# Optimization experiments

Hardware: AMD Instinct MI355X
Metric: run time of the kernel (lower is better)

The kernel has to match this reference:

```python
import jax, jax.numpy as jnp
import numpy as np

N_HEAD = 16
N_KV = 4
HEAD_DIM = 128
EPS = 1e-6


def setup_inputs() -> dict:
    key = jax.random.key(0)
    k1, k2, k3 = jax.random.split(key, 3)
    d_model = N_HEAD * HEAD_DIM
    qkv_out = (N_HEAD + 2 * N_KV) * HEAD_DIM
    B, T = 2, 2048
    x = jax.random.normal(k1, (B, T, d_model), dtype=jnp.float32)
    W_qkv = jax.random.normal(k2, (d_model, qkv_out), dtype=jnp.float32) * (d_model ** -0.5)
    W_proj = jax.random.normal(k3, (d_model, d_model), dtype=jnp.float32) * (d_model ** -0.5)
    q_scale = jnp.ones((HEAD_DIM,), dtype=jnp.float32)
    k_scale = jnp.ones((HEAD_DIM,), dtype=jnp.float32)
    return {"x": x, "W_qkv": W_qkv, "W_proj": W_proj, "q_scale": q_scale, "k_scale": k_scale}


def _rms_norm(t):
    return t * jax.lax.rsqrt(jnp.mean(t * t, axis=-1, keepdims=True) + EPS)


def reference(x, W_qkv, W_proj, q_scale, k_scale):
    B, T, C = x.shape
    qkv = x @ W_qkv  # [B, T, (H+2*KV)*D]
    q, k, v = jnp.split(qkv, [N_HEAD * HEAD_DIM, (N_HEAD + N_KV) * HEAD_DIM], axis=-1)
    q = q.reshape(B, T, N_HEAD, HEAD_DIM).transpose(0, 2, 1, 3)  # [B,H,T,D]
    k = k.reshape(B, T, N_KV, HEAD_DIM).transpose(0, 2, 1, 3)    # [B,KV,T,D]
    v = v.reshape(B, T, N_KV, HEAD_DIM).transpose(0, 2, 1, 3)
    # QK RMS-norm with learned per-dim scales
    q = _rms_norm(q) * q_scale
    k = _rms_norm(k) * k_scale
    # GQA: repeat kv heads to match query heads
    rep = N_HEAD // N_KV
    k = jnp.repeat(k, rep, axis=1)
    v = jnp.repeat(v, rep, axis=1)
    # causal SDPA
    scale = 1.0 / jnp.sqrt(jnp.float32(HEAD_DIM))
    scores = jnp.einsum('bhqd,bhkd->bhqk', q, k) * scale
    causal = jnp.tril(jnp.ones((T, T), dtype=bool))
    scores = jnp.where(causal, scores, jnp.finfo(scores.dtype).min)
    attn = jax.nn.softmax(scores, axis=-1)
    y = jnp.einsum('bhqk,bhkd->bhqd', attn, v)  # [B,H,T,D]
    y = y.transpose(0, 2, 1, 3).reshape(B, T, C)
    return y @ W_proj
```

## Files before the change

### kernel.cpp

```cpp
#include <hip/hip_runtime.h>

typedef __bf16 bf16;
typedef __bf16 bf16x8 __attribute__((ext_vector_type(8)));
typedef __bf16 bf16x4 __attribute__((ext_vector_type(4)));
typedef float f32x4 __attribute__((ext_vector_type(4)));
typedef float f32x16 __attribute__((ext_vector_type(16)));
typedef unsigned u32x4 __attribute__((ext_vector_type(4)));

#define EXP2F(x) __builtin_amdgcn_exp2f(x)

#define LOAD_LDS16(gp, lp)                                                     \
  __builtin_amdgcn_global_load_lds(                                            \
      (const __attribute__((address_space(1))) void*)(gp),                     \
      (__attribute__((address_space(3))) void*)(lp), 16, 0, 0)

__global__ __launch_bounds__(256) void k_cvt_x(const float* __restrict__ in,
                                               bf16* __restrict__ out, int n4) {
  int i = blockIdx.x * 256 + threadIdx.x;
  if (i < n4) {
    float4 v = ((const float4*)in)[i];
    bf16x4 o = {(bf16)v.x, (bf16)v.y, (bf16)v.z, (bf16)v.w};
    ((bf16x4*)out)[i] = o;
  }
}

__global__ __launch_bounds__(256) void k_transpose(const float* __restrict__ in,
                                                   bf16* __restrict__ out,
                                                   int R, int C) {
  __shared__ bf16 t[64 * 65];
  int tid = threadIdx.x;
  int c0 = blockIdx.x * 64, r0 = blockIdx.y * 64;
#pragma unroll
  for (int i = 0; i < 16; ++i) {
    int f = i * 256 + tid;
    int rl = f >> 6, cl = f & 63;
    t[rl * 65 + cl] = (bf16)in[(size_t)(r0 + rl) * C + c0 + cl];
  }
  __syncthreads();
#pragma unroll
  for (int i = 0; i < 16; ++i) {
    int f = i * 256 + tid;
    int cl = f >> 6, rl = f & 63;
    out[(size_t)(c0 + cl) * R + r0 + rl] = t[rl * 65 + cl];
  }
}

template <typename OutT, int BM>
__global__ __launch_bounds__(512, 2) void k_gemm256(const bf16* __restrict__ A,
                                                    const bf16* __restrict__ Bt,
                                                    OutT* __restrict__ C,
                                                    int M, int N, int K) {
  constexpr int ASZ = 4 * BM * 8;
  constexpr int MREP = BM / 32;
  __shared__ alignas(16) bf16 As[2][2][ASZ];
  __shared__ alignas(16) bf16 Bs[2][2][4 * 256 * 8];
  int tid = threadIdx.x;
  int wid = tid >> 6, lane = tid & 63;
  int g = lane >> 4, lr = lane & 15;
  int wrow = (wid >> 2) * (BM / 2), wcol = (wid & 3) * 64;
  int gx = gridDim.x;
  int flat = blockIdx.y * gx + blockIdx.x;
  int cpx = (gx * gridDim.y) >> 3;
  int f2 = (flat & 7) * cpx + (flat >> 3);
  int row0 = (f2 % gx) * BM, col0 = (f2 / gx) * 256;
  int NT = K >> 6;
  f32x4 acc[MREP][4] = {};

  auto stageA = [&](int buf, int kh, int kt) {
#pragma unroll
    for (int pass = 0; pass < BM / 128; ++pass) {
      int slot = pass * 512 + tid;
      int kseg, row;
      if constexpr (BM == 256) { kseg = slot >> 8; row = slot & 255; }
      else { kseg = slot >> 7; row = slot & 127; }
      LOAD_LDS16(A + (size_t)(row0 + row) * K + kt * 64 + kh * 32 + kseg * 8,
                 &As[buf][kh][slot * 8]);
    }
  };
  auto stageB = [&](int buf, int kh, int kt) {
#pragma unroll
    for (int pass = 0; pass < 2; ++pass) {
      int slot = pass * 512 + tid;
      int kseg = slot >> 8, row = slot & 255;
      LOAD_LDS16(Bt + (size_t)(col0 + row) * K + kt * 64 + kh * 32 + kseg * 8,
                 &Bs[buf][kh][slot * 8]);
    }
  };
  auto dsA = [&](int buf, int s, int mq, bf16x8* af) {
#pragma unroll
    for (int i = 0; i < 4; ++i)
      af[i] = *(const bf16x8*)&As[buf][s]
                  [(g * BM + wrow + (mq * 4 + i) * 16 + lr) * 8];
  };
  auto dsB = [&](int buf, int s, bf16x8* bfr) {
#pragma unroll
    for (int i = 0; i < 4; ++i)
      bfr[i] = *(const bf16x8*)&Bs[buf][s][((g << 8) + wcol + i * 16 + lr) * 8];
  };
  auto mfma16 = [&](int mq, bf16x8* af, bf16x8* bfr) {
    __builtin_amdgcn_s_setprio(1);
#pragma unroll
    for (int i = 0; i < 4; ++i)
#pragma unroll
      for (int n = 0; n < 4; ++n)
        acc[mq * 4 + i][n] = __builtin_amdgcn_mfma_f32_16x16x32_bf16(
            af[i], bfr[n], acc[mq * 4 + i][n], 0, 0, 0);
    __builtin_amdgcn_s_setprio(0);
  };

  stageA(0, 0, 0);
  stageB(0, 0, 0);
  stageA(0, 1, 0);
  stageB(0, 1, 0);
  if constexpr (BM == 256)
    asm volatile("s_waitcnt vmcnt(4)" ::: "memory");
  else
    asm volatile("s_waitcnt vmcnt(3)" ::: "memory");
  __builtin_amdgcn_s_barrier();

  for (int T = 0; T < NT; ++T) {
    int buf = T & 1, nbuf = buf ^ 1;
    bool more = (T + 1 < NT);
    bf16x8 af[4], bfr[4];
    if constexpr (BM == 256) {
      dsA(buf, 0, 0, af);
      dsB(buf, 0, bfr);
      if (more) stageA(nbuf, 0, T + 1);
      __builtin_amdgcn_s_barrier();
      mfma16(0, af, bfr);
      __builtin_amdgcn_s_barrier();
      dsA(buf, 0, 1, af);
      if (more) {
        stageB(nbuf, 0, T + 1);
        asm volatile("s_waitcnt vmcnt(4)" ::: "memory");
      } else {
        asm volatile("s_waitcnt vmcnt(0)" ::: "memory");
      }
      __builtin_amdgcn_s_barrier();
      mfma16(1, af, bfr);
      __builtin_amdgcn_s_barrier();
      dsA(buf, 1, 0, af);
      dsB(buf, 1, bfr);
      if (more) stageA(nbuf, 1, T + 1);
      __builtin_amdgcn_s_barrier();
      mfma16(0, af, bfr);
      __builtin_amdgcn_s_barrier();
      dsA(buf, 1, 1, af);
      if (more) {
        stageB(nbuf, 1, T + 1);
        asm volatile("s_waitcnt vmcnt(4)" ::: "memory");
      }
      __builtin_amdgcn_s_barrier();
      mfma16(1, af, bfr);
      __builtin_amdgcn_s_barrier();
    } else {
      dsA(buf, 0, 0, af);
      dsB(buf, 0, bfr);
      if (more) {
        stageA(nbuf, 0, T + 1);
        stageB(nbuf, 0, T + 1);
        asm volatile("s_waitcnt vmcnt(3)" ::: "memory");
      } else {
        asm volatile("s_waitcnt vmcnt(0)" ::: "memory");
      }
      __builtin_amdgcn_s_barrier();
      mfma16(0, af, bfr);
      __builtin_amdgcn_s_barrier();
      dsA(buf, 1, 0, af);
      dsB(buf, 1, bfr);
      if (more) {
        stageA(nbuf, 1, T + 1);
        stageB(nbuf, 1, T + 1);
        asm volatile("s_waitcnt vmcnt(3)" ::: "memory");
      }
      __builtin_amdgcn_s_barrier();
      mfma16(0, af, bfr);
      __builtin_amdgcn_s_barrier();
    }
  }

#pragma unroll
  for (int mi = 0; mi < MREP; ++mi)
#pragma unroll
    for (int ni = 0; ni < 4; ++ni) {
      int rb = row0 + wrow + mi * 16 + g * 4;
      int cc = col0 + wcol + ni * 16 + lr;
#pragma unroll
      for (int r = 0; r < 4; ++r) C[(size_t)(rb + r) * N + cc] = (OutT)acc[mi][ni][r];
    }
}

__global__ __launch_bounds__(256) void k_qknorm(bf16* __restrict__ qkv,
                                                const float* __restrict__ qs,
                                                const float* __restrict__ ks) {
  int tok = blockIdx.x;
  int wid = threadIdx.x >> 6, lane = threadIdx.x & 63;
  int d = lane * 2;
  bf16* rowp = qkv + (size_t)tok * 3072;
#pragma unroll
  for (int i = 0; i < 5; ++i) {
    int cb = (i < 4) ? (wid + i * 4) * 128 : 2048 + wid * 128;
    float v0 = (float)rowp[cb + d], v1 = (float)rowp[cb + d + 1];
    float ss = v0 * v0 + v1 * v1;
#pragma unroll
    for (int off = 1; off < 64; off <<= 1) ss += __shfl_xor(ss, off);
    float r = rsqrtf(ss * (1.0f / 128.0f) + 1e-6f);
    float s0, s1, extra;
    if (i < 4) {
      s0 = qs[d]; s1 = qs[d + 1];
      extra = 0.08838834764831845f * 1.4426950408889634f;
    } else {
      s0 = ks[d]; s1 = ks[d + 1]; extra = 1.0f;
    }
    rowp[cb + d] = (bf16)(v0 * r * s0 * extra);
    rowp[cb + d + 1] = (bf16)(v1 * r * s1 * extra);
  }
}

__global__ __launch_bounds__(256) void k_vt(const bf16* __restrict__ qkv,
                                            bf16* __restrict__ Vt) {
  __shared__ bf16 t[64 * 65];
  int tid = threadIdx.x;
  int t0 = blockIdx.x * 64, d0 = blockIdx.y * 64;
  int bh = blockIdx.z;
  int b = bh >> 2, kvh = bh & 3;
  const bf16* src = qkv + (size_t)(b * 2048) * 3072 + 2560 + kvh * 128;
  bf16* dst = Vt + (size_t)bh * 262144 + (size_t)(t0 >> 6) * 8192;
#pragma unroll
  for (int i = 0; i < 16; ++i) {
    int f = i * 256 + tid;
    int tl = f >> 6, dl = f & 63;
    t[tl * 65 + dl] = src[(size_t)(t0 + tl) * 3072 + d0 + dl];
  }
  __syncthreads();
#pragma unroll
  for (int i = 0; i < 2; ++i) {
    int v = i * 256 + tid;
    int c = v >> 6, dv = v & 63;
    bf16x8 o;
#pragma unroll
    for (int j = 0; j < 8; ++j) o[j] = t[(c * 8 + j) * 65 + dv];
    *(bf16x8*)&dst[(size_t)c * 1024 + (size_t)(d0 + dv) * 8] = o;
  }
}

__device__ inline unsigned pack2bf(float a, float b) {
  union { bf16 h[2]; unsigned u; } x;
  x.h[0] = (bf16)a;
  x.h[1] = (bf16)b;
  return x.u;
}

__global__ __launch_bounds__(256, 2) void k_attn(const bf16* __restrict__ qkv,
                                                 const bf16* __restrict__ Vt,
                                                 bf16* __restrict__ y) {
  int flat = blockIdx.x;
  int slot = flat >> 8;
  int j = flat & 255;
  int xcd = j & 7, iw = j >> 3;
  int h = xcd + 8 * (iw & 1);
  int r = iw >> 1;
  int b = r & 1;
  int qt = slot ? (r >> 1) : (15 - (r >> 1));
  int kvh = h >> 2;
  int tid = threadIdx.x;
  int wid = tid >> 6, lane = tid & 63;
  int qc = lane & 31, hi = lane >> 5;
  __shared__ alignas(16) bf16 Ks[2][16 * 64 * 8];
  __shared__ alignas(16) bf16 Vs[2][8 * 128 * 8];
  const bf16* Qb = qkv + (size_t)(b * 2048) * 3072 + h * 128;
  const bf16* Kb = qkv + (size_t)(b * 2048) * 3072 + 2048 + kvh * 128;
  const bf16* Vb = Vt + (size_t)(b * 4 + kvh) * 262144;
  int qw0 = qt * 128 + wid * 32;
  int qg = qw0 + qc;
  bf16x8 qf[8];
#pragma unroll
  for (int s = 0; s < 8; ++s)
    qf[s] = *(const bf16x8*)&Qb[(size_t)qg * 3072 + s * 16 + hi * 8];
  f32x16 acc[4] = {};
  float mrun = -1e30f, lrun = 0.f;

  auto STAGE = [&](int buf, int kt2) {
    int s0 = kt2 * 64;
#pragma unroll
    for (int i = 0; i < 4; ++i) {
      int sl = i * 256 + tid;
      int ch = sl >> 6, row = sl & 63;
      LOAD_LDS16(Kb + (size_t)(s0 + row) * 3072 + ch * 8, &Ks[buf][sl * 8]);
    }
#pragma unroll
    for (int i = 0; i < 4; ++i) {
      int sl = i * 256 + tid;
      LOAD_LDS16(Vb + (size_t)kt2 * 8192 + sl * 8, &Vs[buf][sl * 8]);
    }
  };

  STAGE(0, 0);
  int cur = 0;
  int ktmax = 2 * qt + 1;
  for (int kt = 0; kt <= ktmax; ++kt) {
    int s0 = kt * 64;
    if (kt < ktmax) {
      STAGE(cur ^ 1, kt + 1);
      asm volatile("s_waitcnt vmcnt(8)" ::: "memory");
    } else {
      asm volatile("s_waitcnt vmcnt(0)" ::: "memory");
    }
    __builtin_amdgcn_s_barrier();
    __builtin_amdgcn_sched_barrier(0);
    if (s0 <= qw0 + 31) {
      f32x16 sc[2] = {};
#pragma unroll
      for (int s = 0; s < 8; ++s)
#pragma unroll
        for (int n = 0; n < 2; ++n) {
          bf16x8 kf =
              *(const bf16x8*)&Ks[cur][(((2 * s + hi) << 6) + n * 32 + qc) * 8];
          sc[n] =
              __builtin_amdgcn_mfma_f32_32x32x16_bf16(kf, qf[s], sc[n], 0, 0, 0);
        }
      if (s0 + 63 > qw0) {
#pragma unroll
        for (int n = 0; n < 2; ++n)
#pragma unroll
          for (int r2 = 0; r2 < 16; ++r2) {
            int kg = s0 + n * 32 + (r2 & 3) + 8 * (r2 >> 2) + 4 * hi;
            if (kg > qg) sc[n][r2] = -1e30f;
          }
      }
      float pm = -1e30f;
#pragma unroll
      for (int n = 0; n < 2; ++n)
#pragma unroll
        for (int r2 = 0; r2 < 16; ++r2) pm = fmaxf(pm, sc[n][r2]);
      pm = fmaxf(pm, __shfl_xor(pm, 32));
      if (__any(pm > mrun + 11.0f)) {
        float mnew = fmaxf(mrun, pm);
        float scl = EXP2F(mrun - mnew);
        mrun = mnew;
        lrun *= scl;
        float sv[16];
#pragma unroll
        for (int r2 = 0; r2 < 16; ++r2)
          sv[r2] = __shfl(scl, (r2 & 3) + 8 * (r2 >> 2) + 4 * hi);
#pragma unroll
        for (int dt = 0; dt < 4; ++dt)
#pragma unroll
          for (int r2 = 0; r2 < 16; ++r2) acc[dt][r2] *= sv[r2];
      }
      float rs = 0.f;
#pragma unroll
      for (int n = 0; n < 2; ++n) {
        unsigned pk[8];
#pragma unroll
        for (int mm = 0; mm < 8; ++mm) {
          float e0 = EXP2F(sc[n][2 * mm] - mrun);
          float e1 = EXP2F(sc[n][2 * mm + 1] - mrun);
          rs += e0 + e1;
          pk[mm] = pack2bf(e0, e1);
        }
#pragma unroll
        for (int l2 = 0; l2 < 2; ++l2) {
          unsigned a0 = pk[4 * l2 + 0], b0 = pk[4 * l2 + 2];
          unsigned a1 = pk[4 * l2 + 1], b1 = pk[4 * l2 + 3];
          asm volatile("v_permlane32_swap_b32 %0, %1" : "+v"(a0), "+v"(b0));
          asm volatile("v_permlane32_swap_b32 %0, %1" : "+v"(a1), "+v"(b1));
          u32x4 w = {a0, a1, b0, b1};
          bf16x8 pf = __builtin_bit_cast(bf16x8, w);
          int c = 2 * (2 * n + l2) + hi;
#pragma unroll
          for (int dt = 0; dt < 4; ++dt) {
            bf16x8 vf =
                *(const bf16x8*)&Vs[cur][((c << 7) + dt * 32 + qc) * 8];
            acc[dt] =
                __builtin_amdgcn_mfma_f32_32x32x16_bf16(pf, vf, acc[dt], 0, 0, 0);
          }
        }
      }
      rs += __shfl_xor(rs, 32);
      lrun += rs;
    }
    __builtin_amdgcn_sched_barrier(0);
    __builtin_amdgcn_s_barrier();
    cur ^= 1;
  }
  float rlv = 1.0f / lrun;
  float rcl[16];
#pragma unroll
  for (int r2 = 0; r2 < 16; ++r2)
    rcl[r2] = __shfl(rlv, (r2 & 3) + 8 * (r2 >> 2) + 4 * hi);
#pragma unroll
  for (int dt = 0; dt < 4; ++dt)
#pragma unroll
    for (int r2 = 0; r2 < 16; ++r2) {
      int row = qw0 + (r2 & 3) + 8 * (r2 >> 2) + 4 * hi;
      float v = acc[dt][r2] * rcl[r2];
      y[(size_t)(b * 2048 + row) * 2048 + h * 128 + dt * 32 + qc] = (bf16)v;
    }
}

extern "C" void kernel_launch(void* const* d_in, const int* in_sizes, int n_in,
                              void* d_out, int out_size, void* d_ws,
                              size_t ws_size, hipStream_t stream) {
  const float* x = (const float*)d_in[0];
  const float* Wqkv = (const float*)d_in[1];
  const float* Wproj = (const float*)d_in[2];
  const float* qs = (const float*)d_in[3];
  const float* ks = (const float*)d_in[4];
  float* out = (float*)d_out;
  char* ws = (char*)d_ws;

  bf16* xb = (bf16*)(ws);
  bf16* Wqkvt = (bf16*)(ws + (size_t)(16u << 20));
  bf16* Wprojt = (bf16*)(ws + (size_t)(28u << 20));
  bf16* qkv = (bf16*)(ws + (size_t)(36u << 20));
  bf16* Vt = Wqkvt;
  bf16* y = xb;

  k_cvt_x<<<8192, 256, 0, stream>>>(x, xb, 8388608 / 4);
  k_transpose<<<dim3(3072 / 64, 2048 / 64), 256, 0, stream>>>(Wqkv, Wqkvt, 2048, 3072);
  k_transpose<<<dim3(2048 / 64, 2048 / 64), 256, 0, stream>>>(Wproj, Wprojt, 2048, 2048);
  k_gemm256<bf16, 256><<<dim3(16, 12), 512, 0, stream>>>(xb, Wqkvt, qkv, 4096, 3072, 2048);
  k_qknorm<<<4096, 256, 0, stream>>>(qkv, qs, ks);
  k_vt<<<dim3(32, 2, 8), 256, 0, stream>>>(qkv, Vt);
  k_attn<<<dim3(512, 1, 1), 256, 0, stream>>>(qkv, Vt, y);
  k_gemm256<float, 128><<<dim3(32, 8), 512, 0, stream>>>(y, Wprojt, out, 4096, 2048, 2048);
}
```

Before: 250.9 us.

## Schedule attention tiles through an atomic work queue, longest first

The static block-to-tile mapping in the causal attention kernel is replaced by a persistent loop. Each block takes the next (query tile, head, batch) item from a global atomic counter, and items are ordered from the largest causal query tile down. This is meant to balance the uneven causal workload dynamically across CUs. In exchange it adds a memset launch, an atomic and a barrier per item, and it drops the earlier XCD-aware head placement that kept K/V reuse local to each L2.

```diff
diff --git a/kernel.cpp b/kernel.cpp
--- a/kernel.cpp
+++ b/kernel.cpp
@@ -253,150 +253,154 @@
 
 __global__ __launch_bounds__(256, 2) void k_attn(const bf16* __restrict__ qkv,
                                                  const bf16* __restrict__ Vt,
-                                                 bf16* __restrict__ y) {
-  int flat = blockIdx.x;
-  int slot = flat >> 8;
-  int j = flat & 255;
-  int xcd = j & 7, iw = j >> 3;
-  int h = xcd + 8 * (iw & 1);
-  int r = iw >> 1;
-  int b = r & 1;
-  int qt = slot ? (r >> 1) : (15 - (r >> 1));
-  int kvh = h >> 2;
+                                                 bf16* __restrict__ y,
+                                                 int* __restrict__ wq) {
   int tid = threadIdx.x;
   int wid = tid >> 6, lane = tid & 63;
   int qc = lane & 31, hi = lane >> 5;
   __shared__ alignas(16) bf16 Ks[2][16 * 64 * 8];
   __shared__ alignas(16) bf16 Vs[2][8 * 128 * 8];
-  const bf16* Qb = qkv + (size_t)(b * 2048) * 3072 + h * 128;
-  const bf16* Kb = qkv + (size_t)(b * 2048) * 3072 + 2048 + kvh * 128;
-  const bf16* Vb = Vt + (size_t)(b * 4 + kvh) * 262144;
-  int qw0 = qt * 128 + wid * 32;
-  int qg = qw0 + qc;
-  bf16x8 qf[8];
-#pragma unroll
-  for (int s = 0; s < 8; ++s)
-    qf[s] = *(const bf16x8*)&Qb[(size_t)qg * 3072 + s * 16 + hi * 8];
-  f32x16 acc[4] = {};
-  float mrun = -1e30f, lrun = 0.f;
-
-  auto STAGE = [&](int buf, int kt2) {
-    int s0 = kt2 * 64;
-#pragma unroll
-    for (int i = 0; i < 4; ++i) {
-      int sl = i * 256 + tid;
-      int ch = sl >> 6, row = sl & 63;
-      LOAD_LDS16(Kb + (size_t)(s0 + row) * 3072 + ch * 8, &Ks[buf][sl * 8]);
-    }
-#pragma unroll
-    for (int i = 0; i < 4; ++i) {
-      int sl = i * 256 + tid;
-      LOAD_LDS16(Vb + (size_t)kt2 * 8192 + sl * 8, &Vs[buf][sl * 8]);
-    }
-  };
-
-  STAGE(0, 0);
-  int cur = 0;
-  int ktmax = 2 * qt + 1;
-  for (int kt = 0; kt <= ktmax; ++kt) {
-    int s0 = kt * 64;
-    if (kt < ktmax) {
-      STAGE(cur ^ 1, kt + 1);
-      asm volatile("s_waitcnt vmcnt(8)" ::: "memory");
-    } else {
-      asm volatile("s_waitcnt vmcnt(0)" ::: "memory");
-    }
-    __builtin_amdgcn_s_barrier();
-    __builtin_amdgcn_sched_barrier(0);
-    if (s0 <= qw0 + 31) {
-      f32x16 sc[2] = {};
-#pragma unroll
-      for (int s = 0; s < 8; ++s)
+  __shared__ int s_item;
+
+  while (true) {
+    if (tid == 0) s_item = atomicAdd(wq, 1);
+    __syncthreads();
+    int item = s_item;
+    if (item >= 512) return;
+    int qt = 15 - (item >> 5);
+    int sub = item & 31;
+    int h = sub & 15, b = sub >> 4;
+    int kvh = h >> 2;
+    const bf16* Qb = qkv + (size_t)(b * 2048) * 3072 + h * 128;
+    const bf16* Kb = qkv + (size_t)(b * 2048) * 3072 + 2048 + kvh * 128;
+    const bf16* Vb = Vt + (size_t)(b * 4 + kvh) * 262144;
+    int qw0 = qt * 128 + wid * 32;
+    int qg = qw0 + qc;
+    bf16x8 qf[8];
+#pragma unroll
+    for (int s = 0; s < 8; ++s)
+      qf[s] = *(const bf16x8*)&Qb[(size_t)qg * 3072 + s * 16 + hi * 8];
+    f32x16 acc[4] = {};
+    float mrun = -1e30f, lrun = 0.f;
+
+    auto STAGE = [&](int buf, int kt2) {
+      int s0 = kt2 * 64;
+#pragma unroll
+      for (int i = 0; i < 4; ++i) {
+        int sl = i * 256 + tid;
+        int ch = sl >> 6, row = sl & 63;
+        LOAD_LDS16(Kb + (size_t)(s0 + row) * 3072 + ch * 8, &Ks[buf][sl * 8]);
+      }
+#pragma unroll
+      for (int i = 0; i < 4; ++i) {
+        int sl = i * 256 + tid;
+        LOAD_LDS16(Vb + (size_t)kt2 * 8192 + sl * 8, &Vs[buf][sl * 8]);
+      }
+    };
+
+    STAGE(0, 0);
+    int cur = 0;
+    int ktmax = 2 * qt + 1;
+    for (int kt = 0; kt <= ktmax; ++kt) {
+      int s0 = kt * 64;
+      if (kt < ktmax) {
+        STAGE(cur ^ 1, kt + 1);
+        asm volatile("s_waitcnt vmcnt(8)" ::: "memory");
+      } else {
+        asm volatile("s_waitcnt vmcnt(0)" ::: "memory");
+      }
+      __builtin_amdgcn_s_barrier();
+      __builtin_amdgcn_sched_barrier(0);
+      if (s0 <= qw0 + 31) {
+        f32x16 sc[2] = {};
+#pragma unroll
+        for (int s = 0; s < 8; ++s)
+#pragma unroll
+          for (int n = 0; n < 2; ++n) {
+            bf16x8 kf = *(const bf16x8*)&Ks[cur]
+                            [(((2 * s + hi) << 6) + n * 32 + qc) * 8];
+            sc[n] = __builtin_amdgcn_mfma_f32_32x32x16_bf16(kf, qf[s], sc[n],
+                                                            0, 0, 0);
+          }
+        if (s0 + 63 > qw0) {
+#pragma unroll
+          for (int n = 0; n < 2; ++n)
+#pragma unroll
+            for (int r2 = 0; r2 < 16; ++r2) {
+              int kg = s0 + n * 32 + (r2 & 3) + 8 * (r2 >> 2) + 4 * hi;
+              if (kg > qg) sc[n][r2] = -1e30f;
+            }
+        }
+        float pm = -1e30f;
+#pragma unroll
+        for (int n = 0; n < 2; ++n)
+#pragma unroll
+          for (int r2 = 0; r2 < 16; ++r2) pm = fmaxf(pm, sc[n][r2]);
+        pm = fmaxf(pm, __shfl_xor(pm, 32));
+        if (__any(pm > mrun + 11.0f)) {
+          float mnew = fmaxf(mrun, pm);
+          float scl = EXP2F(mrun - mnew);
+          mrun = mnew;
+          lrun *= scl;
+          float sv[16];
+#pragma unroll
+          for (int r2 = 0; r2 < 16; ++r2)
+            sv[r2] = __shfl(scl, (r2 & 3) + 8 * (r2 >> 2) + 4 * hi);
+#pragma unroll
+          for (int dt = 0; dt < 4; ++dt)
+#pragma unroll
+            for (int r2 = 0; r2 < 16; ++r2) acc[dt][r2] *= sv[r2];
+        }
+        float rs = 0.f;
 #pragma unroll
         for (int n = 0; n < 2; ++n) {
-          bf16x8 kf =
-              *(const bf16x8*)&Ks[cur][(((2 * s + hi) << 6) + n * 32 + qc) * 8];
-          sc[n] =
-              __builtin_amdgcn_mfma_f32_32x32x16_bf16(kf, qf[s], sc[n], 0, 0, 0);
-        }
-      if (s0 + 63 > qw0) {
-#pragma unroll
-        for (int n = 0; n < 2; ++n)
-#pragma unroll
-          for (int r2 = 0; r2 < 16; ++r2) {
-            int kg = s0 + n * 32 + (r2 & 3) + 8 * (r2 >> 2) + 4 * hi;
-            if (kg > qg) sc[n][r2] = -1e30f;
+          unsigned pk[8];
+#pragma unroll
+          for (int mm = 0; mm < 8; ++mm) {
+            float e0 = EXP2F(sc[n][2 * mm] - mrun);
+            float e1 = EXP2F(sc[n][2 * mm + 1] - mrun);
+            rs += e0 + e1;
+            pk[mm] = pack2bf(e0, e1);
           }
-      }
-      float pm = -1e30f;
-#pragma unroll
-      for (int n = 0; n < 2; ++n)
-#pragma unroll
-        for (int r2 = 0; r2 < 16; ++r2) pm = fmaxf(pm, sc[n][r2]);
-      pm = fmaxf(pm, __shfl_xor(pm, 32));
-      if (__any(pm > mrun + 11.0f)) {
-        float mnew = fmaxf(mrun, pm);
-        float scl = EXP2F(mrun - mnew);
-        mrun = mnew;
-        lrun *= scl;
-        float sv[16];
-#pragma unroll
-        for (int r2 = 0; r2 < 16; ++r2)
-          sv[r2] = __shfl(scl, (r2 & 3) + 8 * (r2 >> 2) + 4 * hi);
-#pragma unroll
-        for (int dt = 0; dt < 4; ++dt)
-#pragma unroll
-          for (int r2 = 0; r2 < 16; ++r2) acc[dt][r2] *= sv[r2];
-      }
-      float rs = 0.f;
-#pragma unroll
-      for (int n = 0; n < 2; ++n) {
-        unsigned pk[8];
-#pragma unroll
-        for (int mm = 0; mm < 8; ++mm) {
-          float e0 = EXP2F(sc[n][2 * mm] - mrun);
-          float e1 = EXP2F(sc[n][2 * mm + 1] - mrun);
-          rs += e0 + e1;
-          pk[mm] = pack2bf(e0, e1);
-        }
-#pragma unroll
-        for (int l2 = 0; l2 < 2; ++l2) {
-          unsigned a0 = pk[4 * l2 + 0], b0 = pk[4 * l2 + 2];
-          unsigned a1 = pk[4 * l2 + 1], b1 = pk[4 * l2 + 3];
-          asm volatile("v_permlane32_swap_b32 %0, %1" : "+v"(a0), "+v"(b0));
-          asm volatile("v_permlane32_swap_b32 %0, %1" : "+v"(a1), "+v"(b1));
-          u32x4 w = {a0, a1, b0, b1};
-          bf16x8 pf = __builtin_bit_cast(bf16x8, w);
-          int c = 2 * (2 * n + l2) + hi;
-#pragma unroll
-          for (int dt = 0; dt < 4; ++dt) {
-            bf16x8 vf =
-                *(const bf16x8*)&Vs[cur][((c << 7) + dt * 32 + qc) * 8];
-            acc[dt] =
-                __builtin_amdgcn_mfma_f32_32x32x16_bf16(pf, vf, acc[dt], 0, 0, 0);
+#pragma unroll
+          for (int l2 = 0; l2 < 2; ++l2) {
+            unsigned a0 = pk[4 * l2 + 0], b0 = pk[4 * l2 + 2];
+            unsigned a1 = pk[4 * l2 + 1], b1 = pk[4 * l2 + 3];
+            asm volatile("v_permlane32_swap_b32 %0, %1" : "+v"(a0), "+v"(b0));
+            asm volatile("v_permlane32_swap_b32 %0, %1" : "+v"(a1), "+v"(b1));
+            u32x4 w = {a0, a1, b0, b1};
+            bf16x8 pf = __builtin_bit_cast(bf16x8, w);
+            int c = 2 * (2 * n + l2) + hi;
+#pragma unroll
+            for (int dt = 0; dt < 4; ++dt) {
+              bf16x8 vf =
+                  *(const bf16x8*)&Vs[cur][((c << 7) + dt * 32 + qc) * 8];
+              acc[dt] = __builtin_amdgcn_mfma_f32_32x32x16_bf16(pf, vf, acc[dt],
+                                                                0, 0, 0);
+            }
           }
         }
-      }
-      rs += __shfl_xor(rs, 32);
-      lrun += rs;
-    }
-    __builtin_amdgcn_sched_barrier(0);
-    __builtin_amdgcn_s_barrier();
-    cur ^= 1;
-  }
-  float rlv = 1.0f / lrun;
-  float rcl[16];
-#pragma unroll
-  for (int r2 = 0; r2 < 16; ++r2)
-    rcl[r2] = __shfl(rlv, (r2 & 3) + 8 * (r2 >> 2) + 4 * hi);
-#pragma unroll
-  for (int dt = 0; dt < 4; ++dt)
-#pragma unroll
-    for (int r2 = 0; r2 < 16; ++r2) {
-      int row = qw0 + (r2 & 3) + 8 * (r2 >> 2) + 4 * hi;
-      float v = acc[dt][r2] * rcl[r2];
-      y[(size_t)(b * 2048 + row) * 2048 + h * 128 + dt * 32 + qc] = (bf16)v;
-    }
+        rs += __shfl_xor(rs, 32);
+        lrun += rs;
+      }
+      __builtin_amdgcn_sched_barrier(0);
+      __builtin_amdgcn_s_barrier();
+      cur ^= 1;
+    }
+    float rlv = 1.0f / lrun;
+    float rcl[16];
+#pragma unroll
+    for (int r2 = 0; r2 < 16; ++r2)
+      rcl[r2] = __shfl(rlv, (r2 & 3) + 8 * (r2 >> 2) + 4 * hi);
+#pragma unroll
+    for (int dt = 0; dt < 4; ++dt)
+#pragma unroll
+      for (int r2 = 0; r2 < 16; ++r2) {
+        int row = qw0 + (r2 & 3) + 8 * (r2 >> 2) + 4 * hi;
+        float v = acc[dt][r2] * rcl[r2];
+        y[(size_t)(b * 2048 + row) * 2048 + h * 128 + dt * 32 + qc] = (bf16)v;
+      }
+  }
 }
 
 extern "C" void kernel_launch(void* const* d_in, const int* in_sizes, int n_in,
@@ -415,6 +419,7 @@
   bf16* Wprojt = (bf16*)(ws + (size_t)(28u << 20));
   bf16* qkv = (bf16*)(ws + (size_t)(36u << 20));
   bf16* Vt = Wqkvt;
+  int* wq = (int*)(ws + (size_t)(24u << 20));
   bf16* y = xb;
 
   k_cvt_x<<<8192, 256, 0, stream>>>(x, xb, 8388608 / 4);
@@ -423,6 +428,7 @@
   k_gemm256<bf16, 256><<<dim3(16, 12), 512, 0, stream>>>(xb, Wqkvt, qkv, 4096, 3072, 2048);
   k_qknorm<<<4096, 256, 0, stream>>>(qkv, qs, ks);
   k_vt<<<dim3(32, 2, 8), 256, 0, stream>>>(qkv, Vt);
-  k_attn<<<dim3(512, 1, 1), 256, 0, stream>>>(qkv, Vt, y);
+  hipMemsetAsync(wq, 0, 4, stream);
+  k_attn<<<dim3(512, 1, 1), 256, 0, stream>>>(qkv, Vt, y, wq);
   k_gemm256<float, 128><<<dim3(32, 8), 512, 0, stream>>>(y, Wprojt, out, 4096, 2048, 2048);
 }
```

Result: slower. 257.2 us (+2.5%).
